# Performance work log

Measured on AMD Instinct MI355X. Metric: run time of the kernel, lower is better.

The kernel has to match this reference:

```python
import jax, jax.numpy as jnp
import numpy as np

B, I, H = 32768, 256, 512

def setup_inputs() -> dict:
    key = jax.random.key(0)
    ks = jax.random.split(key, 12)
    s_lstm = 1.0 / np.sqrt(H)
    inp = {
        "inputs": jax.random.normal(ks[0], (B, I), dtype=jnp.float32),
        "h0": jax.random.normal(ks[1], (B, H), dtype=jnp.float32),
        "c0": jax.random.normal(ks[2], (B, H), dtype=jnp.float32),
        "ts": jax.random.uniform(ks[3], (B, 2), dtype=jnp.float32),
        # LSTMCell params (torch layout: [4H, in], gate order i,f,g,o)
        "W_ih": jax.random.uniform(ks[4], (4 * H, I), minval=-s_lstm, maxval=s_lstm, dtype=jnp.float32),
        "W_hh": jax.random.uniform(ks[5], (4 * H, H), minval=-s_lstm, maxval=s_lstm, dtype=jnp.float32),
        "b_ih": jax.random.uniform(ks[6], (4 * H,), minval=-s_lstm, maxval=s_lstm, dtype=jnp.float32),
        "b_hh": jax.random.uniform(ks[7], (4 * H,), minval=-s_lstm, maxval=s_lstm, dtype=jnp.float32),
        # ODE vector field: Linear(H,H) -> Tanh -> Linear(H,H)
        "W1": jax.random.uniform(ks[8], (H, H), minval=-s_lstm, maxval=s_lstm, dtype=jnp.float32),
        "b1": jax.random.uniform(ks[9], (H,), minval=-s_lstm, maxval=s_lstm, dtype=jnp.float32),
        "W2": jax.random.uniform(ks[10], (H, H), minval=-s_lstm, maxval=s_lstm, dtype=jnp.float32),
        "b2": jax.random.uniform(ks[11], (H,), minval=-s_lstm, maxval=s_lstm, dtype=jnp.float32),
    }
    return inp


def _lstm_cell(x, h, c, W_ih, W_hh, b_ih, b_hh):
    z = x @ W_ih.T + b_ih + h @ W_hh.T + b_hh  # [B, 4H]
    i, f, g, o = jnp.split(z, 4, axis=-1)
    i = jax.nn.sigmoid(i)
    f = jax.nn.sigmoid(f)
    g = jnp.tanh(g)
    o = jax.nn.sigmoid(o)
    c2 = f * c + i * g
    h2 = o * jnp.tanh(c2)
    return h2, c2


def reference(inputs, h0, c0, ts, W_ih, W_hh, b_ih, b_hh, W1, b1, W2, b2):
    # two sequential LSTMCell updates with the same input
    h1, c1 = _lstm_cell(inputs, h0, c0, W_ih, W_hh, b_ih, b_hh)
    new_h, new_c = _lstm_cell(inputs, h1, c1, W_ih, W_hh, b_ih, b_hh)

    # autonomous vector field f(h) = W2 tanh(W1 h + b1) + b2
    def f(h):
        return jnp.tanh(h @ W1.T + b1) @ W2.T + b2

    # batched single RK4 step from ts[:,0] to ts[:,1] (fused over batch)
    dt = (ts[:, 1] - ts[:, 0])[:, None]  # [B,1]
    k1 = f(new_h)
    k2 = f(new_h + 0.5 * dt * k1)
    k3 = f(new_h + 0.5 * dt * k2)
    k4 = f(new_h + dt * k3)
    ht = new_h + (dt / 6.0) * (k1 + 2.0 * k2 + 2.0 * k3 + k4)
    return (ht, new_c)
```

## Files before the change

kernel.cpp:

```cpp
#include <hip/hip_runtime.h>
#include <math.h>

#define BATCH 32768
#define ISZ   256
#define HSZ   512
#define KC    768

typedef __attribute__((ext_vector_type(8))) short bf16x8;
typedef __attribute__((ext_vector_type(4))) float f32x4;

static __device__ unsigned short g_xbf[(size_t)BATCH * ISZ];
static __device__ unsigned short g_ha [(size_t)BATCH * HSZ];
static __device__ unsigned short g_hb [(size_t)BATCH * HSZ];
static __device__ float          g_h2f[(size_t)BATCH * HSZ];
static __device__ unsigned short g_Wc [2048 * KC];
static __device__ unsigned short g_W1p[HSZ * HSZ];
static __device__ unsigned short g_W2p[HSZ * HSZ];

__device__ __forceinline__ unsigned short f2bf(float f) {
    unsigned int u = __float_as_uint(f);
    u += 0x7fff + ((u >> 16) & 1);
    return (unsigned short)(u >> 16);
}
__device__ __forceinline__ float bf2f(unsigned short s) {
    return __uint_as_float((unsigned int)s << 16);
}
__device__ __forceinline__ float fsigm(float x) { return 1.0f / (1.0f + __expf(-x)); }
__device__ __forceinline__ float ftanh(float x) { return 1.0f - 2.0f / (__expf(2.0f * x) + 1.0f); }

__device__ __forceinline__ void gload16(const void* g, void* l) {
    __builtin_amdgcn_global_load_lds(
        (const __attribute__((address_space(1))) unsigned int*)g,
        (__attribute__((address_space(3))) unsigned int*)l, 16, 0, 0);
}

template <int DST>
__global__ __launch_bounds__(256) void conv_kernel(
    const float* __restrict__ src, int nv, int w4shift, int dstride, int doff)
{
    unsigned short* __restrict__ dst = DST == 0 ? g_xbf : DST == 1 ? g_ha : g_Wc;
    int i = blockIdx.x * 256 + threadIdx.x;
    const int gs = gridDim.x * 256;
    for (; i < nv; i += gs) {
        const int r = i >> w4shift;
        const int c = i & ((1 << w4shift) - 1);
        const float4 v = ((const float4*)src)[i];
        ushort4 o;
        o.x = f2bf(v.x); o.y = f2bf(v.y); o.z = f2bf(v.z); o.w = f2bf(v.w);
        *(ushort4*)&dst[(size_t)r * dstride + doff + c * 4] = o;
    }
}

template <int DST>
__global__ __launch_bounds__(256) void conv_fragW(const float* __restrict__ src)
{
    unsigned short* __restrict__ dst = DST == 0 ? g_W1p : g_W2p;
    const int c = blockIdx.x * 256 + threadIdx.x;
    const int l15 = c & 15, lq = (c >> 4) & 3, st = (c >> 6) & 15, fb = c >> 10;
    const int n = fb * 16 + l15;
    const int k = st * 32 + lq * 8;
    const float4 v0 = *(const float4*)&src[(size_t)n * HSZ + k];
    const float4 v1 = *(const float4*)&src[(size_t)n * HSZ + k + 4];
    unsigned short o[8] = {f2bf(v0.x), f2bf(v0.y), f2bf(v0.z), f2bf(v0.w),
                           f2bf(v1.x), f2bf(v1.y), f2bf(v1.z), f2bf(v1.w)};
    *(bf16x8*)&dst[(size_t)c * 8] = *(bf16x8*)o;
}

template <int MODE>
__global__ __launch_bounds__(256) void cell_kernel(
    const float* __restrict__ bih, const float* __restrict__ bhh,
    const float* __restrict__ c_in, float* __restrict__ c_out)
{
    constexpr int NKT = KC / 64;
    constexpr int NCH = 16;

    __shared__ __align__(16) unsigned short As[2][128 * 64];
    __shared__ __align__(16) unsigned short Bs[2][128 * 64];

    const int orig = blockIdx.x;
    const int q = gridDim.x >> 3;
    const int wg = (orig & 7) * q + (orig >> 3);
    const int nbc = wg % NCH;
    const int mBase = (wg / NCH) * 128;

    const int tid  = threadIdx.x;
    const int lane = tid & 63;
    const int wid  = tid >> 6;
    const int wr   = wid >> 1, wc = wid & 1;
    const int l15  = lane & 15, lq = lane >> 4;

    const unsigned short* __restrict__ Ah = (MODE == 0) ? g_ha : g_hb;

    const int arow = tid >> 3, ch = tid & 7;
    int bgrow[4];
#pragma unroll
    for (int j = 0; j < 4; ++j) {
        const int vr = j * 32 + arow;
        const int g    = (vr >> 4) & 3;
        const int jcol = nbc * 32 + (vr >> 6) * 16 + (vr & 15);
        bgrow[j] = g * 512 + jcol;
    }

    auto stage = [&](int buf, int kt) {
        const int k0 = kt * 64;
#pragma unroll
        for (int j = 0; j < 4; ++j) {
            const int row = j * 32 + arow;
            const unsigned short* ga = (k0 < 256)
                ? g_xbf + (size_t)(mBase + row) * ISZ + (k0       + ch * 8)
                : Ah    + (size_t)(mBase + row) * HSZ + (k0 - 256 + ch * 8);
            gload16(ga, (char*)As[buf] + j * 4096 + wid * 1024);
            const unsigned short* gb = g_Wc + (size_t)bgrow[j] * KC + k0 + ch * 8;
            gload16(gb, (char*)Bs[buf] + j * 4096 + wid * 1024);
        }
    };

    f32x4 acc[4][4];
#pragma unroll
    for (int fm = 0; fm < 4; ++fm)
#pragma unroll
        for (int fn = 0; fn < 4; ++fn) acc[fm][fn] = (f32x4){0.f, 0.f, 0.f, 0.f};

    stage(0, 0);
    int cur = 0;
    for (int kt = 0; kt < NKT; ++kt) {
        if (kt + 1 < NKT) {
            stage(cur ^ 1, kt + 1);
            asm volatile("s_waitcnt vmcnt(8)" ::: "memory");
        } else {
            asm volatile("s_waitcnt vmcnt(0)" ::: "memory");
        }
        asm volatile("s_barrier" ::: "memory");
#pragma unroll
        for (int kk = 0; kk < 2; ++kk) {
            bf16x8 a[4], b[4];
#pragma unroll
            for (int f = 0; f < 4; ++f) {
                const int rowA = wr * 64 + f * 16 + l15;
                a[f] = *(const bf16x8*)((const char*)As[cur] + rowA * 128 + kk * 64 + lq * 16);
                const int rowB = wc * 64 + f * 16 + l15;
                b[f] = *(const bf16x8*)((const char*)Bs[cur] + rowB * 128 + kk * 64 + lq * 16);
            }
#pragma unroll
            for (int fm = 0; fm < 4; ++fm)
#pragma unroll
                for (int fn = 0; fn < 4; ++fn)
                    acc[fm][fn] = __builtin_amdgcn_mfma_f32_16x16x32_bf16(
                        a[fm], b[fn], acc[fm][fn], 0, 0, 0);
        }
        asm volatile("s_barrier" ::: "memory");
        cur ^= 1;
    }

    const int j = nbc * 32 + wc * 16 + l15;
    float bsum[4];
#pragma unroll
    for (int g = 0; g < 4; ++g) bsum[g] = bih[g * 512 + j] + bhh[g * 512 + j];
#pragma unroll
    for (int fm = 0; fm < 4; ++fm) {
#pragma unroll
        for (int r = 0; r < 4; ++r) {
            const int m = mBase + wr * 64 + fm * 16 + lq * 4 + r;
            const size_t idx = (size_t)m * HSZ + j;
            const float ig = fsigm(acc[fm][0][r] + bsum[0]);
            const float fg = fsigm(acc[fm][1][r] + bsum[1]);
            const float gg = ftanh(acc[fm][2][r] + bsum[2]);
            const float og = fsigm(acc[fm][3][r] + bsum[3]);
            const float cnew = fg * c_in[idx] + ig * gg;
            const float hnew = og * ftanh(cnew);
            c_out[idx] = cnew;
            if constexpr (MODE == 0) g_hb[idx] = f2bf(hnew);
            else                     g_h2f[idx] = hnew;
        }
    }
}

__global__ __launch_bounds__(512, 1) void rk_fused_kernel(
    const float* __restrict__ ts, const float* __restrict__ b1,
    const float* __restrict__ b2, float* __restrict__ out_ht)
{
    __shared__ __align__(16) unsigned short sU[32 * 512];
    __shared__ __align__(16) unsigned short sH[32 * 512];
    __shared__ __align__(16) unsigned short sW[8 * 2 * 2048];

    const int tid = threadIdx.x, lane = tid & 63;
    const int w = tid >> 6;
    const int l15 = lane & 15, lq = lane >> 4;
    const int nb = w * 64;
    const int m0 = blockIdx.x * 32;

    float b1v[4], b2v[4];
#pragma unroll
    for (int fn = 0; fn < 4; ++fn) {
        b1v[fn] = b1[nb + fn * 16 + l15];
        b2v[fn] = b2[nb + fn * 16 + l15];
    }

    {
        const float4* __restrict__ src = (const float4*)(g_h2f + (size_t)m0 * HSZ);
#pragma unroll
        for (int i = 0; i < 8; ++i) {
            const int flat = i * 512 + tid;
            const int row = flat >> 7;
            const int c4 = flat & 127;
            const float4 v = src[flat];
            ushort4 o;
            o.x = f2bf(v.x); o.y = f2bf(v.y); o.z = f2bf(v.z); o.w = f2bf(v.w);
            const int off = row * 1024 + ((c4 * 8) ^ ((row & 7) << 4));
            *(ushort4*)((char*)sU + off) = o;
            *(ushort4*)((char*)sH + off) = o;
        }
    }
    __syncthreads();

    f32x4 rk[2][4];
#pragma unroll
    for (int fm = 0; fm < 2; ++fm)
#pragma unroll
        for (int fn = 0; fn < 4; ++fn) rk[fm][fn] = (f32x4){0.f, 0.f, 0.f, 0.f};

    char* const sWme = (char*)sW + w * 8192;
    auto stage_w = [&](const unsigned short* __restrict__ Wp, int st, int buf) {
#pragma unroll
        for (int f = 0; f < 4; ++f) {
            const unsigned short* g =
                Wp + (size_t)(((w * 4 + f) * 16 + st) * 512) + lane * 8;
            gload16(g, sWme + buf * 4096 + f * 1024);
        }
    };
    auto loadA = [&](bf16x8 (&aa)[2], int st) {
#pragma unroll
        for (int f = 0; f < 2; ++f) {
            const int row = f * 16 + l15;
            aa[f] = *(const bf16x8*)((const char*)sU + row * 1024 +
                                     ((st * 64 + lq * 16) ^ ((l15 & 7) << 4)));
        }
    };

    auto do_gemm = [&](const unsigned short* __restrict__ Wp, f32x4 (&gacc)[2][4]) {
#pragma unroll
        for (int fm = 0; fm < 2; ++fm)
#pragma unroll
            for (int fn = 0; fn < 4; ++fn) gacc[fm][fn] = (f32x4){0.f, 0.f, 0.f, 0.f};
        stage_w(Wp, 0, 0);
#pragma unroll 1
        for (int st = 0; st < 16; ++st) {
            if (st < 15) {
                stage_w(Wp, st + 1, (st + 1) & 1);
                asm volatile("s_waitcnt vmcnt(4)" ::: "memory");
            } else {
                asm volatile("s_waitcnt vmcnt(0)" ::: "memory");
            }
            bf16x8 a[2], b[4];
#pragma unroll
            for (int f = 0; f < 4; ++f)
                b[f] = *(const bf16x8*)(sWme + (st & 1) * 4096 + f * 1024 + lane * 16);
            loadA(a, st);
#pragma unroll
            for (int fm = 0; fm < 2; ++fm)
#pragma unroll
                for (int fn = 0; fn < 4; ++fn)
                    gacc[fm][fn] = __builtin_amdgcn_mfma_f32_16x16x32_bf16(
                        a[fm], b[fn], gacc[fm][fn], 0, 0, 0);
        }
    };

#pragma unroll 1
    for (int s = 0; s < 4; ++s) {
        f32x4 gacc[2][4];
        do_gemm(g_W1p, gacc);
        __syncthreads();
#pragma unroll
        for (int fm = 0; fm < 2; ++fm)
#pragma unroll
            for (int fn = 0; fn < 4; ++fn)
#pragma unroll
                for (int r = 0; r < 4; ++r) {
                    const int row = fm * 16 + lq * 4 + r;
                    const int col = nb + fn * 16 + l15;
                    *(unsigned short*)((char*)sU + row * 1024 +
                                       ((col * 2) ^ ((row & 7) << 4))) =
                        f2bf(ftanh(gacc[fm][fn][r] + b1v[fn]));
                }
        __syncthreads();
        do_gemm(g_W2p, gacc);
        __syncthreads();
        const float wk = (s == 1 || s == 2) ? 2.0f : 1.0f;
        const float cs = (s == 2) ? 1.0f : 0.5f;
#pragma unroll
        for (int fm = 0; fm < 2; ++fm) {
            float dtf[4];
#pragma unroll
            for (int r = 0; r < 4; ++r) {
                const int m = m0 + fm * 16 + lq * 4 + r;
                const float2 tv = *(const float2*)&ts[2 * m];
                dtf[r] = tv.y - tv.x;
            }
#pragma unroll
            for (int fn = 0; fn < 4; ++fn)
#pragma unroll
                for (int r = 0; r < 4; ++r) {
                    const int row = fm * 16 + lq * 4 + r;
                    const int col = nb + fn * 16 + l15;
                    const float kv = gacc[fm][fn][r] + b2v[fn];
                    rk[fm][fn][r] += wk * kv;
                    if (s < 3) {
                        const int off = row * 1024 + ((col * 2) ^ ((row & 7) << 4));
                        const float h2 = bf2f(*(const unsigned short*)((const char*)sH + off));
                        *(unsigned short*)((char*)sU + off) = f2bf(h2 + cs * dtf[r] * kv);
                    } else {
                        const size_t idx = (size_t)(m0 + row) * HSZ + col;
                        out_ht[idx] = g_h2f[idx] + dtf[r] * (1.0f / 6.0f) * rk[fm][fn][r];
                    }
                }
        }
        if (s < 3) __syncthreads();
    }
}

extern "C" void kernel_launch(void* const* d_in, const int* in_sizes, int n_in,
                              void* d_out, int out_size, void* d_ws, size_t ws_size,
                              hipStream_t stream) {
    const float* x   = (const float*)d_in[0];
    const float* h0  = (const float*)d_in[1];
    const float* c0  = (const float*)d_in[2];
    const float* ts  = (const float*)d_in[3];
    const float* Wih = (const float*)d_in[4];
    const float* Whh = (const float*)d_in[5];
    const float* bih = (const float*)d_in[6];
    const float* bhh = (const float*)d_in[7];
    const float* W1  = (const float*)d_in[8];
    const float* b1  = (const float*)d_in[9];
    const float* W2  = (const float*)d_in[10];
    const float* b2  = (const float*)d_in[11];

    float* out_ht = (float*)d_out;
    float* out_c  = out_ht + (size_t)BATCH * HSZ;

    dim3 blk(256);
    conv_kernel<0><<<2048, blk, 0, stream>>>(x,   BATCH * ISZ / 4, 6, ISZ, 0);
    conv_kernel<1><<<2048, blk, 0, stream>>>(h0,  BATCH * HSZ / 4, 7, HSZ, 0);
    conv_kernel<2><<<256,  blk, 0, stream>>>(Wih, 2048 * 256 / 4,  6, KC, 0);
    conv_kernel<2><<<256,  blk, 0, stream>>>(Whh, 2048 * 512 / 4,  7, KC, 256);
    conv_fragW<0><<<128,  blk, 0, stream>>>(W1);
    conv_fragW<1><<<128,  blk, 0, stream>>>(W2);

    dim3 gcell(BATCH / 128 * 16);

    cell_kernel<0><<<gcell, blk, 0, stream>>>(bih, bhh, c0,    out_c);
    cell_kernel<1><<<gcell, blk, 0, stream>>>(bih, bhh, out_c, out_c);

    rk_fused_kernel<<<BATCH / 32, 512, 0, stream>>>(ts, b1, b2, out_ht);
}
```

Baseline: 771.4 us.

## Store second LSTM h in bf16, keep RK base in registers, triple-buffer weights

The second LSTM step now writes h as bf16 into an existing buffer instead of an fp32 scratch array. The RK kernel reads it directly into shared memory and keeps the per-thread h values packed in registers, which removes the sH shared buffer and the fp32 re-read in the final output. Weight staging now moves in half-tiles through a three-slot ring with MFMA priority raised, to overlap loads with compute at lower LDS cost. The tradeoff is that the final ht is built from a bf16-rounded h instead of the fp32 h, which reduces accuracy.

```diff
diff --git a/kernel.cpp b/kernel.cpp
--- a/kernel.cpp
+++ b/kernel.cpp
@@ -12,7 +12,6 @@
 static __device__ unsigned short g_xbf[(size_t)BATCH * ISZ];
 static __device__ unsigned short g_ha [(size_t)BATCH * HSZ];
 static __device__ unsigned short g_hb [(size_t)BATCH * HSZ];
-static __device__ float          g_h2f[(size_t)BATCH * HSZ];
 static __device__ unsigned short g_Wc [2048 * KC];
 static __device__ unsigned short g_W1p[HSZ * HSZ];
 static __device__ unsigned short g_W2p[HSZ * HSZ];
@@ -170,7 +169,7 @@
             const float hnew = og * ftanh(cnew);
             c_out[idx] = cnew;
             if constexpr (MODE == 0) g_hb[idx] = f2bf(hnew);
-            else                     g_h2f[idx] = hnew;
+            else                     g_ha[idx] = f2bf(hnew);
         }
     }
 }
@@ -180,8 +179,7 @@
     const float* __restrict__ b2, float* __restrict__ out_ht)
 {
     __shared__ __align__(16) unsigned short sU[32 * 512];
-    __shared__ __align__(16) unsigned short sH[32 * 512];
-    __shared__ __align__(16) unsigned short sW[8 * 2 * 2048];
+    __shared__ __align__(16) unsigned short sW[8 * 3 * 1024];
 
     const int tid = threadIdx.x, lane = tid & 63;
     const int w = tid >> 6;
@@ -197,20 +195,29 @@
     }
 
     {
-        const float4* __restrict__ src = (const float4*)(g_h2f + (size_t)m0 * HSZ);
-#pragma unroll
-        for (int i = 0; i < 8; ++i) {
+#pragma unroll
+        for (int i = 0; i < 4; ++i) {
             const int flat = i * 512 + tid;
-            const int row = flat >> 7;
-            const int c4 = flat & 127;
-            const float4 v = src[flat];
-            ushort4 o;
-            o.x = f2bf(v.x); o.y = f2bf(v.y); o.z = f2bf(v.z); o.w = f2bf(v.w);
-            const int off = row * 1024 + ((c4 * 8) ^ ((row & 7) << 4));
-            *(ushort4*)((char*)sU + off) = o;
-            *(ushort4*)((char*)sH + off) = o;
-        }
-    }
+            const int row = flat >> 6;
+            const int c16 = flat & 63;
+            const uint4 v = *(const uint4*)(g_ha + (size_t)(m0 + row) * HSZ + c16 * 8);
+            *(uint4*)((char*)sU + row * 1024 + ((c16 * 16) ^ ((row & 7) << 4))) = v;
+        }
+    }
+
+    unsigned int h2p[2][4][2];
+#pragma unroll
+    for (int fm = 0; fm < 2; ++fm)
+#pragma unroll
+        for (int fn = 0; fn < 4; ++fn)
+#pragma unroll
+            for (int rr = 0; rr < 2; ++rr) {
+                const int col = nb + fn * 16 + l15;
+                const unsigned int lo = g_ha[(size_t)(m0 + fm * 16 + lq * 4 + rr * 2)     * HSZ + col];
+                const unsigned int hi = g_ha[(size_t)(m0 + fm * 16 + lq * 4 + rr * 2 + 1) * HSZ + col];
+                h2p[fm][fn][rr] = lo | (hi << 16);
+            }
+    asm volatile("s_waitcnt vmcnt(0)" ::: "memory");
     __syncthreads();
 
     f32x4 rk[2][4];
@@ -219,13 +226,15 @@
 #pragma unroll
         for (int fn = 0; fn < 4; ++fn) rk[fm][fn] = (f32x4){0.f, 0.f, 0.f, 0.f};
 
-    char* const sWme = (char*)sW + w * 8192;
-    auto stage_w = [&](const unsigned short* __restrict__ Wp, int st, int buf) {
-#pragma unroll
-        for (int f = 0; f < 4; ++f) {
-            const unsigned short* g =
-                Wp + (size_t)(((w * 4 + f) * 16 + st) * 512) + lane * 8;
-            gload16(g, sWme + buf * 4096 + f * 1024);
+    char* const sWme = (char*)sW + w * 6144;
+
+    auto stage_half = [&](const unsigned short* __restrict__ Wp, int hh) {
+        const int st = hh >> 1, half = hh & 1, buf = hh % 3;
+#pragma unroll
+        for (int f = 0; f < 2; ++f) {
+            const int fb = w * 4 + half * 2 + f;
+            const unsigned short* g = Wp + (size_t)((fb * 16 + st) * 512) + lane * 8;
+            gload16(g, sWme + buf * 2048 + f * 1024);
         }
     };
     auto loadA = [&](bf16x8 (&aa)[2], int st) {
@@ -242,26 +251,33 @@
         for (int fm = 0; fm < 2; ++fm)
 #pragma unroll
             for (int fn = 0; fn < 4; ++fn) gacc[fm][fn] = (f32x4){0.f, 0.f, 0.f, 0.f};
-        stage_w(Wp, 0, 0);
+        stage_half(Wp, 0);
+        stage_half(Wp, 1);
+        bf16x8 a[2];
 #pragma unroll 1
-        for (int st = 0; st < 16; ++st) {
-            if (st < 15) {
-                stage_w(Wp, st + 1, (st + 1) & 1);
+        for (int hh = 0; hh < 32; ++hh) {
+            if (hh < 30) {
+                stage_half(Wp, hh + 2);
                 asm volatile("s_waitcnt vmcnt(4)" ::: "memory");
+            } else if (hh == 30) {
+                asm volatile("s_waitcnt vmcnt(2)" ::: "memory");
             } else {
                 asm volatile("s_waitcnt vmcnt(0)" ::: "memory");
             }
-            bf16x8 a[2], b[4];
-#pragma unroll
-            for (int f = 0; f < 4; ++f)
-                b[f] = *(const bf16x8*)(sWme + (st & 1) * 4096 + f * 1024 + lane * 16);
-            loadA(a, st);
-#pragma unroll
-            for (int fm = 0; fm < 2; ++fm)
-#pragma unroll
-                for (int fn = 0; fn < 4; ++fn)
-                    gacc[fm][fn] = __builtin_amdgcn_mfma_f32_16x16x32_bf16(
-                        a[fm], b[fn], gacc[fm][fn], 0, 0, 0);
+            if (!(hh & 1)) loadA(a, hh >> 1);
+            const char* bp = sWme + (hh % 3) * 2048;
+            bf16x8 bfr0 = *(const bf16x8*)(bp + lane * 16);
+            bf16x8 bfr1 = *(const bf16x8*)(bp + 1024 + lane * 16);
+            const int f0 = (hh & 1) * 2;
+            __builtin_amdgcn_s_setprio(1);
+#pragma unroll
+            for (int fm = 0; fm < 2; ++fm) {
+                gacc[fm][f0]     = __builtin_amdgcn_mfma_f32_16x16x32_bf16(
+                    a[fm], bfr0, gacc[fm][f0], 0, 0, 0);
+                gacc[fm][f0 + 1] = __builtin_amdgcn_mfma_f32_16x16x32_bf16(
+                    a[fm], bfr1, gacc[fm][f0 + 1], 0, 0, 0);
+            }
+            __builtin_amdgcn_s_setprio(0);
         }
     };
 
@@ -304,13 +320,14 @@
                     const int col = nb + fn * 16 + l15;
                     const float kv = gacc[fm][fn][r] + b2v[fn];
                     rk[fm][fn][r] += wk * kv;
+                    const float h2 = bf2f((unsigned short)
+                        (h2p[fm][fn][r >> 1] >> ((r & 1) * 16)));
                     if (s < 3) {
                         const int off = row * 1024 + ((col * 2) ^ ((row & 7) << 4));
-                        const float h2 = bf2f(*(const unsigned short*)((const char*)sH + off));
                         *(unsigned short*)((char*)sU + off) = f2bf(h2 + cs * dtf[r] * kv);
                     } else {
-                        const size_t idx = (size_t)(m0 + row) * HSZ + col;
-                        out_ht[idx] = g_h2f[idx] + dtf[r] * (1.0f / 6.0f) * rk[fm][fn][r];
+                        out_ht[(size_t)(m0 + row) * HSZ + col] =
+                            h2 + dtf[r] * (1.0f / 6.0f) * rk[fm][fn][r];
                     }
                 }
         }
```

Result: slower. 2.583 ms (+234.8%).
